# Kernel tuning notes

Hardware: AMD Instinct MI355X
Metric: run time of the kernel (lower is better)

Reference implementation:

```python
import jax, jax.numpy as jnp
import numpy as np

N = 100000
E = 3200000
IN_F = 256
OUT_F = 256


def setup_inputs() -> dict:
    key = jax.random.key(0)
    k1, k2, k3, k4, k5 = jax.random.split(key, 5)
    stdv = 1.0 / np.sqrt(OUT_F)
    x = jax.random.normal(k1, (N, IN_F), dtype=jnp.float32)
    edge_index = jax.random.randint(k2, (2, E), 0, N, dtype=jnp.int64)
    edge_weight = jax.random.uniform(k3, (E,), dtype=jnp.float32)
    weight = jax.random.uniform(k4, (IN_F, OUT_F), dtype=jnp.float32, minval=-stdv, maxval=stdv)
    bias = jax.random.uniform(k5, (OUT_F,), dtype=jnp.float32, minval=-stdv, maxval=stdv)
    return {"x": x, "edge_index": edge_index, "edge_weight": edge_weight,
            "weight": weight, "bias": bias}


def reference(x, edge_index, edge_weight, weight, bias):
    # Dense transform: [N, in] @ [in, out] -> [N, out]
    support = x @ weight
    row, col = edge_index[0], edge_index[1]
    # SpMM: out[row] += edge_weight * support[col]
    messages = edge_weight[:, None] * support[col]  # [E, out]
    output = jax.ops.segment_sum(messages, row, num_segments=N)  # [N, out]
    return output + bias
```

## Files before the change

kernel.cpp:

```cpp
#include <hip/hip_runtime.h>
#include <hip/hip_fp16.h>

#define IN_F 256
#define OUT_F 256
#define HALF_F 128
#define RPB_SHIFT 9
#define RPB (1 << RPB_SHIFT)
#define NBINS_MAX 256
#define TILE_E 4096
#define XS_PAD 40

using bf16x8 = __attribute__((ext_vector_type(8))) short;
using f32x4  = __attribute__((ext_vector_type(4))) float;
using ull    = unsigned long long;

__device__ inline short bf16rne(float f) {
    unsigned u = __float_as_uint(f);
    u = u + 0x7FFFu + ((u >> 16) & 1u);
    return (short)(u >> 16);
}
__device__ inline unsigned pack_half2(float a, float b) {
    __half2 h = __floats2half2_rn(a, b);
    return *reinterpret_cast<unsigned*>(&h);
}

__global__ __launch_bounds__(256) void convert_wt_kernel(
    const float* __restrict__ w, short* __restrict__ wt)
{
    const int idx = blockIdx.x * blockDim.x + threadIdx.x;
    const int c = idx >> 8, k = idx & 255;
    wt[(size_t)c * IN_F + k] = bf16rne(w[(size_t)k * OUT_F + c]);
}

__global__ __launch_bounds__(256) void mfma_gemm_kernel(
    const float* __restrict__ x, const short* __restrict__ wt,
    __half* __restrict__ supA, __half* __restrict__ supB, int M)
{
    __shared__ short xs[2][64][XS_PAD];

    const int t    = threadIdx.x;
    const int lane = t & 63;
    const int wid  = t >> 6;
    const int l15  = lane & 15;
    const int l4   = lane >> 4;
    const int rowbase = blockIdx.x * 64;
    const int cbase   = wid * 64;

    const int srow = t >> 2;
    const int sks  = (t & 3) * 8;
    int grow = rowbase + srow; if (grow > M - 1) grow = M - 1;
    const float* xsrc = x + (size_t)grow * IN_F + sks;

    f32x4 acc[4][4];
#pragma unroll
    for (int rt = 0; rt < 4; ++rt)
#pragma unroll
        for (int ct = 0; ct < 4; ++ct)
            acc[rt][ct] = (f32x4){0.f, 0.f, 0.f, 0.f};

    const short* wp[4];
#pragma unroll
    for (int ct = 0; ct < 4; ++ct)
        wp[ct] = wt + (size_t)(cbase + ct * 16 + l15) * IN_F + l4 * 8;

    {
        const float4 f0 = *(const float4*)(xsrc + 0);
        const float4 f1 = *(const float4*)(xsrc + 4);
        bf16x8 v;
        v[0] = bf16rne(f0.x); v[1] = bf16rne(f0.y);
        v[2] = bf16rne(f0.z); v[3] = bf16rne(f0.w);
        v[4] = bf16rne(f1.x); v[5] = bf16rne(f1.y);
        v[6] = bf16rne(f1.z); v[7] = bf16rne(f1.w);
        *(bf16x8*)&xs[0][srow][sks] = v;
    }
    __syncthreads();

#pragma unroll
    for (int k0 = 0; k0 < 8; ++k0) {
        const int cur = k0 & 1;

        float4 nf0, nf1;
        if (k0 < 7) {
            nf0 = *(const float4*)(xsrc + (k0 + 1) * 32);
            nf1 = *(const float4*)(xsrc + (k0 + 1) * 32 + 4);
        }

        bf16x8 b[4];
#pragma unroll
        for (int ct = 0; ct < 4; ++ct)
            b[ct] = *(const bf16x8*)(wp[ct] + k0 * 32);

        bf16x8 a[4];
#pragma unroll
        for (int rt = 0; rt < 4; ++rt)
            a[rt] = *(const bf16x8*)&xs[cur][rt * 16 + l15][l4 * 8];

#pragma unroll
        for (int rt = 0; rt < 4; ++rt)
#pragma unroll
            for (int ct = 0; ct < 4; ++ct)
                acc[rt][ct] = __builtin_amdgcn_mfma_f32_16x16x32_bf16(
                    b[ct], a[rt], acc[rt][ct], 0, 0, 0);

        if (k0 < 7) {
            bf16x8 v;
            v[0] = bf16rne(nf0.x); v[1] = bf16rne(nf0.y);
            v[2] = bf16rne(nf0.z); v[3] = bf16rne(nf0.w);
            v[4] = bf16rne(nf1.x); v[5] = bf16rne(nf1.y);
            v[6] = bf16rne(nf1.z); v[7] = bf16rne(nf1.w);
            *(bf16x8*)&xs[cur ^ 1][srow][sks] = v;
        }
        __syncthreads();
    }

    __half* dst = (wid < 2) ? supA : supB;
    const int fbase = (wid & 1) * 64;
#pragma unroll
    for (int rt = 0; rt < 4; ++rt) {
        const int r = rowbase + rt * 16 + l15;
        if (r >= M) continue;
#pragma unroll
        for (int ct = 0; ct < 4; ++ct) {
            uint2 pk;
            pk.x = pack_half2(acc[rt][ct][0], acc[rt][ct][1]);
            pk.y = pack_half2(acc[rt][ct][2], acc[rt][ct][3]);
            *(uint2*)(dst + (size_t)r * HALF_F + fbase + ct * 16 + l4 * 4) = pk;
        }
    }
}

__global__ __launch_bounds__(256) void a1a_hist_kernel(
    const int* __restrict__ ei, int* __restrict__ thist, int E)
{
    __shared__ int hist[NBINS_MAX];
    const int tid = threadIdx.x;
    hist[tid] = 0;
    __syncthreads();
    const int base = blockIdx.x * TILE_E;
#pragma unroll
    for (int i = 0; i < TILE_E / 256; ++i) {
        const int e = base + i * 256 + tid;
        if (e < E)
            atomicAdd(&hist[__builtin_nontemporal_load(ei + e) >> RPB_SHIFT], 1);
    }
    __syncthreads();
    thist[(size_t)blockIdx.x * NBINS_MAX + tid] = hist[tid];
}

__global__ __launch_bounds__(256) void tile_scan_kernel(
    int* __restrict__ thist, int* __restrict__ btot, int T)
{
    const int b   = blockIdx.x;
    const int tid = threadIdx.x;
    __shared__ int s[256];
    int carry = 0;
    for (int c0 = 0; c0 < T; c0 += 256) {
        const int t = c0 + tid;
        const int v = (t < T) ? thist[(size_t)t * NBINS_MAX + b] : 0;
        s[tid] = v;
        __syncthreads();
        for (int d = 1; d < 256; d <<= 1) {
            const int u = (tid >= d) ? s[tid - d] : 0;
            __syncthreads();
            s[tid] += u;
            __syncthreads();
        }
        const int total = s[255];
        if (t < T) thist[(size_t)t * NBINS_MAX + b] = carry + s[tid] - v;
        carry += total;
        __syncthreads();
    }
    if (tid == 0) btot[b] = carry;
}

__global__ __launch_bounds__(NBINS_MAX) void bin_scan_kernel(
    const int* __restrict__ btot, int* __restrict__ bstart, int nbins)
{
    __shared__ int s[NBINS_MAX];
    const int tid = threadIdx.x;
    const int v = (tid < nbins) ? btot[tid] : 0;
    s[tid] = v;
    __syncthreads();
    for (int d = 1; d < NBINS_MAX; d <<= 1) {
        const int u = (tid >= d) ? s[tid - d] : 0;
        __syncthreads();
        s[tid] += u;
        __syncthreads();
    }
    bstart[tid] = s[tid] - v;
}

__global__ __launch_bounds__(256) void a1b_scatter_kernel(
    const int* __restrict__ ei, const float* __restrict__ ew,
    const int* __restrict__ bstart, const int* __restrict__ thist,
    ull* __restrict__ tscw, int E)
{
    __shared__ int hist[NBINS_MAX];
    __shared__ int rbase[NBINS_MAX];
    const int tid = threadIdx.x;
    hist[tid]  = 0;
    rbase[tid] = bstart[tid] + thist[(size_t)blockIdx.x * NBINS_MAX + tid];
    __syncthreads();
    const int base = blockIdx.x * TILE_E;
#pragma unroll
    for (int i = 0; i < TILE_E / 256; ++i) {
        const int e = base + i * 256 + tid;
        if (e < E) {
            const int      row = __builtin_nontemporal_load(ei + e);
            const int      col = __builtin_nontemporal_load(ei + E + e);
            const unsigned wb  = __builtin_nontemporal_load((const unsigned*)ew + e);
            const int b   = row >> RPB_SHIFT;
            const int rnk = atomicAdd(&hist[b], 1);
            tscw[rbase[b] + rnk] = ((ull)wb << 32) |
                                   ((unsigned)col << RPB_SHIFT) |
                                   (unsigned)(row & (RPB - 1));
        }
    }
}

__global__ __launch_bounds__(256) void a2_sort_kernel(
    const ull* __restrict__ tscw, const int* __restrict__ bstart,
    const int* __restrict__ btot, int* __restrict__ counts,
    int* __restrict__ cursor, ull* __restrict__ scw, int M)
{
    const int b   = blockIdx.x;
    const int tid = threadIdx.x;
    const int n   = btot[b];
    const int s0  = bstart[b];

    __shared__ int hist[RPB];
    __shared__ int cur[RPB];
    __shared__ int s[256];

    hist[tid] = 0; hist[tid + 256] = 0;
    __syncthreads();

    for (int i = tid; i < n; i += 256)
        atomicAdd(&hist[(int)(__builtin_nontemporal_load(tscw + s0 + i) & (RPB - 1))], 1);
    __syncthreads();

    const int h0 = hist[2 * tid], h1 = hist[2 * tid + 1];
    const int own = h0 + h1;
    s[tid] = own;
    __syncthreads();
    for (int d = 1; d < 256; d <<= 1) {
        const int u = (tid >= d) ? s[tid - d] : 0;
        __syncthreads();
        s[tid] += u;
        __syncthreads();
    }
    const int excl = s[tid] - own;

    const int r0 = (b << RPB_SHIFT) + 2 * tid, r1 = r0 + 1;
    cur[2 * tid]     = s0 + excl;
    cur[2 * tid + 1] = s0 + excl + h0;
    if (r0 < M) { counts[r0] = h0; cursor[r0] = s0 + excl; }
    if (r1 < M) { counts[r1] = h1; cursor[r1] = s0 + excl + h0; }
    __syncthreads();

    for (int i = tid; i < n; i += 256) {
        const ull en = __builtin_nontemporal_load(tscw + s0 + i);
        const int pos = atomicAdd(&cur[(int)(en & (RPB - 1))], 1);
        scw[pos] = (en & 0xFFFFFFFF00000000ull) |
                   (unsigned)((en >> RPB_SHIFT) & 0x1FFFFu);
    }
}

__global__ __launch_bounds__(256) void pull_half_kernel(
    const int* __restrict__ counts, const int* __restrict__ cursor,
    const ull* __restrict__ scw, const __half* __restrict__ suph,
    const float* __restrict__ biash, float* __restrict__ outh, int M)
{
    const int wv  = blockIdx.x * 4 + (threadIdx.x >> 6);
    const int row = wv * 2 + ((threadIdx.x >> 5) & 1);
    if (row >= M) return;
    const int l = threadIdx.x & 31;

    const int cnt   = counts[row];
    const int start = cursor[row];

    float4 acc = *(const float4*)(biash + l * 4);

#define GATHER_FMA_H(pe)                                                      \
    {                                                                         \
        const int   c  = (int)(unsigned)(pe);                                 \
        const float wj = __uint_as_float((unsigned)((pe) >> 32));             \
        const uint2 v = *(const uint2*)(suph + (size_t)c * HALF_F + l * 4);   \
        const float2 f0 = __half22float2(*(const __half2*)&v.x);              \
        const float2 f1 = __half22float2(*(const __half2*)&v.y);              \
        acc.x = fmaf(wj, f0.x, acc.x); acc.y = fmaf(wj, f0.y, acc.y);         \
        acc.z = fmaf(wj, f1.x, acc.z); acc.w = fmaf(wj, f1.y, acc.w);         \
    }

    for (int j0 = 0; j0 < cnt; j0 += 32) {
        ull pr = 0ull;
        if (j0 + l < cnt)
            pr = __builtin_nontemporal_load(scw + start + j0 + l);
        const int m = min(32, cnt - j0);

        int j = 0;
        for (; j + 4 <= m; j += 4) {
            const ull p0 = __shfl(pr, j, 32),     p1 = __shfl(pr, j + 1, 32);
            const ull p2 = __shfl(pr, j + 2, 32), p3 = __shfl(pr, j + 3, 32);
            GATHER_FMA_H(p0); GATHER_FMA_H(p1);
            GATHER_FMA_H(p2); GATHER_FMA_H(p3);
        }
        for (; j < m; ++j) {
            const ull p = __shfl(pr, j, 32);
            GATHER_FMA_H(p);
        }
    }
#undef GATHER_FMA_H

    f32x4 o; o[0] = acc.x; o[1] = acc.y; o[2] = acc.z; o[3] = acc.w;
    __builtin_nontemporal_store(o, (f32x4*)(outh + (size_t)row * OUT_F + l * 4));
}

__global__ __launch_bounds__(256) void bias_init_kernel(
    float* __restrict__ out, const float* __restrict__ bias, int total4)
{
    const float4* b4 = (const float4*)bias;
    float4* o4 = (float4*)out;
    for (int i = blockIdx.x * blockDim.x + threadIdx.x; i < total4;
         i += gridDim.x * blockDim.x)
        o4[i] = b4[i & 63];
}

__global__ __launch_bounds__(256) void edge_scatter_kernel(
    const int* __restrict__ ei, const float* __restrict__ ew,
    const __half* __restrict__ supA, const __half* __restrict__ supB,
    float* __restrict__ out, int E)
{
    const int e = blockIdx.x * 4 + (threadIdx.x >> 6);
    if (e >= E) return;
    const int lane = threadIdx.x & 63;
    const int   row = ei[e];
    const int   col = ei[E + e];
    const float wgt = ew[e];
    const __half* src = (lane < 32) ? supA : supB;
    const int fl = (lane & 31) * 4;
    const uint2 v = *(const uint2*)(src + (size_t)col * HALF_F + fl);
    const float2 f0 = __half22float2(*(const __half2*)&v.x);
    const float2 f1 = __half22float2(*(const __half2*)&v.y);
    float* o = out + (size_t)row * OUT_F + (lane >> 5) * HALF_F + fl;
    unsafeAtomicAdd(o + 0, wgt * f0.x);
    unsafeAtomicAdd(o + 1, wgt * f0.y);
    unsafeAtomicAdd(o + 2, wgt * f1.x);
    unsafeAtomicAdd(o + 3, wgt * f1.y);
}

extern "C" void kernel_launch(void* const* d_in, const int* in_sizes, int n_in,
                              void* d_out, int out_size, void* d_ws, size_t ws_size,
                              hipStream_t stream)
{
    const float* x    = (const float*)d_in[0];
    const int*   ei   = (const int*)d_in[1];
    const float* ew   = (const float*)d_in[2];
    const float* w    = (const float*)d_in[3];
    const float* bias = (const float*)d_in[4];
    float* out = (float*)d_out;

    const int M = in_sizes[0] / IN_F;
    const int E = in_sizes[2];
    const int nbins = (M + RPB - 1) >> RPB_SHIFT;
    const int T     = (E + TILE_E - 1) / TILE_E;

    char* p = (char*)d_ws;
    const size_t suph_b   = (((size_t)M * HALF_F * sizeof(__half)) + 255) & ~255ull;
    const size_t counts_b = ((size_t)M * 4 + 255) & ~255ull;
    const size_t btot_b   = NBINS_MAX * 4;
    const size_t cursor_b = counts_b;
    const size_t bstart_b = NBINS_MAX * 4;
    const size_t thist_b  = (((size_t)T * NBINS_MAX * 4) + 255) & ~255ull;
    const size_t scw_b    = ((size_t)E * 8 + 255) & ~255ull;
    const size_t tscw_b   = scw_b;
    const size_t wt_b     = (size_t)IN_F * OUT_F * sizeof(short);
    const size_t need     = 2 * suph_b + counts_b + btot_b + cursor_b + bstart_b
                          + thist_b + scw_b + tscw_b + wt_b;

    __half* supA   = (__half*)p;               p += suph_b;
    __half* supB   = (__half*)p;               p += suph_b;
    int*    counts = (int*)p;                  p += counts_b;
    int*    btot   = (int*)p;                  p += btot_b;
    int*    cursor = (int*)p;                  p += cursor_b;
    int*    bstart = (int*)p;                  p += bstart_b;
    int*    thist  = (int*)p;                  p += thist_b;
    ull*    scw    = (ull*)p;                  p += scw_b;
    ull*    tscw   = (ull*)p;                  p += tscw_b;
    short*  wtb    = (short*)p;

    convert_wt_kernel<<<(IN_F * OUT_F) / 256, 256, 0, stream>>>(w, wtb);
    mfma_gemm_kernel<<<(M + 63) / 64, 256, 0, stream>>>(x, wtb, supA, supB, M);

    if (ws_size >= need) {
        a1a_hist_kernel<<<T, 256, 0, stream>>>(ei, thist, E);
        tile_scan_kernel<<<nbins, 256, 0, stream>>>(thist, btot, T);
        bin_scan_kernel<<<1, NBINS_MAX, 0, stream>>>(btot, bstart, nbins);
        a1b_scatter_kernel<<<T, 256, 0, stream>>>(ei, ew, bstart, thist, tscw, E);
        a2_sort_kernel<<<nbins, 256, 0, stream>>>(
            tscw, bstart, btot, counts, cursor, scw, M);
        const int pblocks = ((M + 1) / 2 + 3) / 4;
        pull_half_kernel<<<pblocks, 256, 0, stream>>>(
            counts, cursor, scw, supA, bias, out, M);
        pull_half_kernel<<<pblocks, 256, 0, stream>>>(
            counts, cursor, scw, supB, bias + HALF_F, out + HALF_F, M);
    } else {
        const int total4 = M * OUT_F / 4;
        bias_init_kernel<<<2048, 256, 0, stream>>>(out, bias, total4);
        edge_scatter_kernel<<<(E + 3) / 4, 256, 0, stream>>>(ei, ew, supA, supB, out, E);
    }
}
```

Before: 413.2 us.

## Sort each row's edges by column shard and shrink GEMM row tile

The per-bin sort now keys edges on (row, column shard of 16K nodes), so each row's edge list is grouped by source-column region. The intent is better cache locality when the pull kernels gather support rows. Separately, the GEMM block tile shrinks from 64 to 32 rows, which doubles the block count and lowers per-thread accumulator registers, at the cost of more reloads of the weight operand. The sort uses 8x larger shared-memory histograms and a longer serial scan per thread.

```diff
diff --git a/kernel.cpp b/kernel.cpp
--- a/kernel.cpp
+++ b/kernel.cpp
@@ -9,8 +9,10 @@
 #define NBINS_MAX 256
 #define TILE_E 4096
 #define XS_PAD 40
+#define SHARD_SHIFT 14
 
 using bf16x8 = __attribute__((ext_vector_type(8))) short;
+using bf16x4 = __attribute__((ext_vector_type(4))) short;
 using f32x4  = __attribute__((ext_vector_type(4))) float;
 using ull    = unsigned long long;
 
@@ -36,24 +38,24 @@
     const float* __restrict__ x, const short* __restrict__ wt,
     __half* __restrict__ supA, __half* __restrict__ supB, int M)
 {
-    __shared__ short xs[2][64][XS_PAD];
+    __shared__ short xs[2][32][XS_PAD];
 
     const int t    = threadIdx.x;
     const int lane = t & 63;
     const int wid  = t >> 6;
     const int l15  = lane & 15;
     const int l4   = lane >> 4;
-    const int rowbase = blockIdx.x * 64;
+    const int rowbase = blockIdx.x * 32;
     const int cbase   = wid * 64;
 
-    const int srow = t >> 2;
-    const int sks  = (t & 3) * 8;
+    const int srow = t >> 3;
+    const int sks  = (t & 7) * 4;
     int grow = rowbase + srow; if (grow > M - 1) grow = M - 1;
     const float* xsrc = x + (size_t)grow * IN_F + sks;
 
-    f32x4 acc[4][4];
-#pragma unroll
-    for (int rt = 0; rt < 4; ++rt)
+    f32x4 acc[2][4];
+#pragma unroll
+    for (int rt = 0; rt < 2; ++rt)
 #pragma unroll
         for (int ct = 0; ct < 4; ++ct)
             acc[rt][ct] = (f32x4){0.f, 0.f, 0.f, 0.f};
@@ -64,14 +66,11 @@
         wp[ct] = wt + (size_t)(cbase + ct * 16 + l15) * IN_F + l4 * 8;
 
     {
-        const float4 f0 = *(const float4*)(xsrc + 0);
-        const float4 f1 = *(const float4*)(xsrc + 4);
-        bf16x8 v;
-        v[0] = bf16rne(f0.x); v[1] = bf16rne(f0.y);
-        v[2] = bf16rne(f0.z); v[3] = bf16rne(f0.w);
-        v[4] = bf16rne(f1.x); v[5] = bf16rne(f1.y);
-        v[6] = bf16rne(f1.z); v[7] = bf16rne(f1.w);
-        *(bf16x8*)&xs[0][srow][sks] = v;
+        const float4 f = *(const float4*)xsrc;
+        bf16x4 v;
+        v[0] = bf16rne(f.x); v[1] = bf16rne(f.y);
+        v[2] = bf16rne(f.z); v[3] = bf16rne(f.w);
+        *(bf16x4*)&xs[0][srow][sks] = v;
     }
     __syncthreads();
 
@@ -79,36 +78,31 @@
     for (int k0 = 0; k0 < 8; ++k0) {
         const int cur = k0 & 1;
 
-        float4 nf0, nf1;
-        if (k0 < 7) {
-            nf0 = *(const float4*)(xsrc + (k0 + 1) * 32);
-            nf1 = *(const float4*)(xsrc + (k0 + 1) * 32 + 4);
-        }
+        float4 nf;
+        if (k0 < 7) nf = *(const float4*)(xsrc + (k0 + 1) * 32);
 
         bf16x8 b[4];
 #pragma unroll
         for (int ct = 0; ct < 4; ++ct)
             b[ct] = *(const bf16x8*)(wp[ct] + k0 * 32);
 
-        bf16x8 a[4];
-#pragma unroll
-        for (int rt = 0; rt < 4; ++rt)
+        bf16x8 a[2];
+#pragma unroll
+        for (int rt = 0; rt < 2; ++rt)
             a[rt] = *(const bf16x8*)&xs[cur][rt * 16 + l15][l4 * 8];
 
 #pragma unroll
-        for (int rt = 0; rt < 4; ++rt)
+        for (int rt = 0; rt < 2; ++rt)
 #pragma unroll
             for (int ct = 0; ct < 4; ++ct)
                 acc[rt][ct] = __builtin_amdgcn_mfma_f32_16x16x32_bf16(
                     b[ct], a[rt], acc[rt][ct], 0, 0, 0);
 
         if (k0 < 7) {
-            bf16x8 v;
-            v[0] = bf16rne(nf0.x); v[1] = bf16rne(nf0.y);
-            v[2] = bf16rne(nf0.z); v[3] = bf16rne(nf0.w);
-            v[4] = bf16rne(nf1.x); v[5] = bf16rne(nf1.y);
-            v[6] = bf16rne(nf1.z); v[7] = bf16rne(nf1.w);
-            *(bf16x8*)&xs[cur ^ 1][srow][sks] = v;
+            bf16x4 v;
+            v[0] = bf16rne(nf.x); v[1] = bf16rne(nf.y);
+            v[2] = bf16rne(nf.z); v[3] = bf16rne(nf.w);
+            *(bf16x4*)&xs[cur ^ 1][srow][sks] = v;
         }
         __syncthreads();
     }
@@ -116,7 +110,7 @@
     __half* dst = (wid < 2) ? supA : supB;
     const int fbase = (wid & 1) * 64;
 #pragma unroll
-    for (int rt = 0; rt < 4; ++rt) {
+    for (int rt = 0; rt < 2; ++rt) {
         const int r = rowbase + rt * 16 + l15;
         if (r >= M) continue;
 #pragma unroll
@@ -228,20 +222,27 @@
     const int n   = btot[b];
     const int s0  = bstart[b];
 
-    __shared__ int hist[RPB];
-    __shared__ int cur[RPB];
+    __shared__ int hcur[RPB * 8];
+    __shared__ int hbase[RPB * 8];
     __shared__ int s[256];
 
-    hist[tid] = 0; hist[tid + 256] = 0;
-    __syncthreads();
-
-    for (int i = tid; i < n; i += 256)
-        atomicAdd(&hist[(int)(__builtin_nontemporal_load(tscw + s0 + i) & (RPB - 1))], 1);
-    __syncthreads();
-
-    const int h0 = hist[2 * tid], h1 = hist[2 * tid + 1];
-    const int own = h0 + h1;
-    s[tid] = own;
+#pragma unroll
+    for (int k = 0; k < 16; ++k) hcur[tid + k * 256] = 0;
+    __syncthreads();
+
+    for (int i = tid; i < n; i += 256) {
+        const ull en = __builtin_nontemporal_load(tscw + s0 + i);
+        const int key = ((int)(en & (RPB - 1)) << 3) |
+                        (int)((en >> (RPB_SHIFT + SHARD_SHIFT)) & 7u);
+        atomicAdd(&hcur[key], 1);
+    }
+    __syncthreads();
+
+    int loc[16];
+    int run = 0;
+#pragma unroll
+    for (int k = 0; k < 16; ++k) { loc[k] = hcur[tid * 16 + k]; run += loc[k]; }
+    s[tid] = run;
     __syncthreads();
     for (int d = 1; d < 256; d <<= 1) {
         const int u = (tid >= d) ? s[tid - d] : 0;
@@ -249,18 +250,29 @@
         s[tid] += u;
         __syncthreads();
     }
-    const int excl = s[tid] - own;
-
-    const int r0 = (b << RPB_SHIFT) + 2 * tid, r1 = r0 + 1;
-    cur[2 * tid]     = s0 + excl;
-    cur[2 * tid + 1] = s0 + excl + h0;
-    if (r0 < M) { counts[r0] = h0; cursor[r0] = s0 + excl; }
-    if (r1 < M) { counts[r1] = h1; cursor[r1] = s0 + excl + h0; }
+    int accum = s[tid] - run;
+#pragma unroll
+    for (int k = 0; k < 16; ++k) { hbase[tid * 16 + k] = accum; accum += loc[k]; }
+    __syncthreads();
+
+    {
+        const int r0 = 2 * tid, r1 = r0 + 1;
+        const int st0  = hbase[r0 << 3];
+        const int st1  = hbase[r1 << 3];
+        const int end1 = (r1 == RPB - 1) ? n : hbase[(r1 + 1) << 3];
+        const int gr0 = (b << RPB_SHIFT) + r0, gr1 = gr0 + 1;
+        if (gr0 < M) { counts[gr0] = st1 - st0;  cursor[gr0] = s0 + st0; }
+        if (gr1 < M) { counts[gr1] = end1 - st1; cursor[gr1] = s0 + st1; }
+    }
+#pragma unroll
+    for (int k = 0; k < 16; ++k) hcur[tid * 16 + k] = s0 + hbase[tid * 16 + k];
     __syncthreads();
 
     for (int i = tid; i < n; i += 256) {
         const ull en = __builtin_nontemporal_load(tscw + s0 + i);
-        const int pos = atomicAdd(&cur[(int)(en & (RPB - 1))], 1);
+        const int key = ((int)(en & (RPB - 1)) << 3) |
+                        (int)((en >> (RPB_SHIFT + SHARD_SHIFT)) & 7u);
+        const int pos = atomicAdd(&hcur[key], 1);
         scw[pos] = (en & 0xFFFFFFFF00000000ull) |
                    (unsigned)((en >> RPB_SHIFT) & 0x1FFFFu);
     }
@@ -390,7 +402,7 @@
     short*  wtb    = (short*)p;
 
     convert_wt_kernel<<<(IN_F * OUT_F) / 256, 256, 0, stream>>>(w, wtb);
-    mfma_gemm_kernel<<<(M + 63) / 64, 256, 0, stream>>>(x, wtb, supA, supB, M);
+    mfma_gemm_kernel<<<(M + 31) / 32, 256, 0, stream>>>(x, wtb, supA, supB, M);
 
     if (ws_size >= need) {
         a1a_hist_kernel<<<T, 256, 0, stream>>>(ei, thist, E);
```

Measured after the change: 439.4 us, median of 2. 6.3% more time.
